# Optimization experiments

Measured on AMD Instinct MI355X. Metric: run time of the kernel, lower is better.

The kernel has to match this reference:

```python
import jax, jax.numpy as jnp
import numpy as np

N = 50000      # nodes
E = 800000     # edges (avg degree 16)
IN = 128       # in_features
OUT = 64       # out_features
NEG_SLOPE = 0.2


def setup_inputs() -> dict:
    key = jax.random.key(0)
    ks = jax.random.split(key, 6)
    x = jax.random.normal(ks[0], (N, IN), dtype=jnp.float32)
    edge_src = jax.random.randint(ks[1], (E,), 0, N, dtype=jnp.int32)  # row i of adj
    edge_dst = jax.random.randint(ks[2], (E,), 0, N, dtype=jnp.int32)  # col j of adj
    stdv = 1.0 / np.sqrt(OUT)
    W = jax.random.uniform(ks[3], (IN, OUT), jnp.float32, -stdv, stdv)
    a = jax.random.uniform(ks[4], (2 * OUT, 1), jnp.float32, -stdv, stdv)
    bias = jax.random.uniform(ks[5], (OUT,), jnp.float32, -stdv, stdv)
    return {"x": x, "W": W, "a": a, "bias": bias,
            "edge_src": edge_src, "edge_dst": edge_dst}


def reference(x, W, a, bias, edge_src, edge_dst):
    # h = input @ weight + bias    [N, OUT]
    h = x @ W + bias
    # Per-node attention halves: Wh1[i] + Wh2[j] == (e = Wh1 + Wh2.T)[i, j]
    Wh1 = h @ a[:OUT, 0]   # [N]
    Wh2 = h @ a[OUT:, 0]   # [N]
    # Edge-centric scores only where adj is nonzero (mirrors e.sparse_mask(adj))
    e = jax.nn.leaky_relu(Wh1[edge_src] + Wh2[edge_dst], NEG_SLOPE)  # [E]
    # Sparse softmax over dim=1 -> segment softmax grouped by source row
    emax = jax.ops.segment_max(e, edge_src, num_segments=N)          # [N]
    ex = jnp.exp(e - emax[edge_src])                                 # [E]
    denom = jax.ops.segment_sum(ex, edge_src, num_segments=N)        # [N]
    alpha = ex / denom[edge_src]                                     # [E]
    # out[i] = sum_j alpha_ij * h[j]  (sparse attention @ h)
    out = jax.ops.segment_sum(alpha[:, None] * h[edge_dst], edge_src,
                              num_segments=N)                        # [N, OUT]
    return out
```

## Files before the change

### kernel.cpp

```cpp
#include <hip/hip_runtime.h>
#include <math.h>


typedef unsigned long long u64;
typedef unsigned int u32;
typedef unsigned short u16;
typedef __attribute__((ext_vector_type(8))) short bf16x8;
typedef __attribute__((ext_vector_type(4))) float f32x4;

namespace {
constexpr int NN   = 50000;
constexpr int EE   = 800000;
constexpr int INF_ = 128;
constexpr int OUTF = 64;
constexpr float NEG_SLOPE = 0.2f;
constexpr int MAXDEG = 64;

constexpr int NBUCK   = 196;
constexpr int BSTRIDE = 16;
constexpr int BCAP    = 4608;
constexpr int S1_CHUNK  = 2048;
constexpr int S1_BLOCKS = (EE + S1_CHUNK - 1) / S1_CHUNK;
constexpr int GEMM_BLOCKS = (NN + 127) / 128;
constexpr int K1_BLOCKS = S1_BLOCKS + GEMM_BLOCKS;
constexpr int AGG_BLOCKS = (NN + 63) / 64;
}

static __device__ __forceinline__ u16 bf16rne(float v) {
    u32 u = __builtin_bit_cast(u32, v);
    return (u16)((u + 0x7fffu + ((u >> 16) & 1u)) >> 16);
}
static __device__ __forceinline__ float bf2f(u16 b) {
    return __builtin_bit_cast(float, (u32)b << 16);
}
static __device__ __forceinline__ u32 pack2bf(float a, float b) {
    return (u32)bf16rne(a) | ((u32)bf16rne(b) << 16);
}

__global__ __launch_bounds__(256)
void gat_fused(const float* __restrict__ x, const float* __restrict__ W,
               const float* __restrict__ av, const float* __restrict__ bias,
               const int* __restrict__ esrc, const int* __restrict__ edst,
               u32* __restrict__ h16, float* __restrict__ wh1,
               float* __restrict__ wh2, int* __restrict__ bcnt_g,
               u64* __restrict__ bdata)
{
    __shared__ u64 smem[4096];
    const int id  = blockIdx.x;
    const int tid = threadIdx.x;
    const int ridx = id >> 1;
    const bool is_gemm = (id & 1) == 0;

    if (!is_gemm) {
        u64* s_pairs = smem;
        int* s_bcnt  = (int*)((char*)smem + 16384);
        int* s_scan  = s_bcnt + NBUCK;
        int* s_goff  = s_scan + NBUCK;

        for (int i = tid; i < NBUCK; i += 256) s_bcnt[i] = 0;
        __syncthreads();

        const int e0  = ridx * S1_CHUNK;
        const int tot = (EE - e0) < S1_CHUNK ? (EE - e0) : S1_CHUNK;

        int mb[8], mp[8]; u64 mv[8]; int nmine = 0;
#pragma unroll
        for (int k = 0; k < 8; ++k) {
            const int e = e0 + tid + k * 256;
            if (e < e0 + tot) {
                const int s = esrc[e], d = edst[e];
                const int b = s >> 8;
                mb[nmine] = b;
                mp[nmine] = atomicAdd(&s_bcnt[b], 1);
                mv[nmine] = ((u64)(u32)d << 32) | (u32)s;
                ++nmine;
            }
        }
        __syncthreads();
        if (tid < NBUCK) s_scan[tid] = s_bcnt[tid];
        __syncthreads();
        for (int off = 1; off < NBUCK; off <<= 1) {
            int v = 0;
            if (tid < NBUCK && tid >= off) v = s_scan[tid - off];
            __syncthreads();
            if (tid < NBUCK && tid >= off) s_scan[tid] += v;
            __syncthreads();
        }
        if (tid < NBUCK) {
            const int c = s_bcnt[tid];
            s_goff[tid] = c > 0 ? atomicAdd(&bcnt_g[tid * BSTRIDE], c) : 0;
        }
        __syncthreads();
        for (int k = 0; k < nmine; ++k) {
            const int b = mb[k];
            s_pairs[s_scan[b] - s_bcnt[b] + mp[k]] = mv[k];
        }
        __syncthreads();
        for (int i = tid; i < tot; i += 256) {
            const u64 p = s_pairs[i];
            const int s = (int)(u32)(p & 0xffffffffull);
            const int b = s >> 8;
            const int g = s_goff[b] + (i - (s_scan[b] - s_bcnt[b]));
            if (g < BCAP) bdata[(size_t)b * BCAP + g] = p;
        }
        return;
    }

    u32* Whi = (u32*)smem;
    u32* Wlo = Whi + 4096;

#pragma unroll
    for (int i = 0; i < 4; ++i) {
        const int idx    = tid * 4 + i;
        const int lane_s = idx & 63;
        const int kt_s   = (idx >> 6) & 3;
        const int nt_s   = idx >> 8;
        const int n  = nt_s * 16 + (lane_s & 15);
        const int k0 = kt_s * 32 + (lane_s >> 4) * 8;
        u32 hw[4], lw[4];
#pragma unroll
        for (int jp = 0; jp < 4; ++jp) {
            const float va = W[(k0 + 2*jp    ) * OUTF + n];
            const float vb = W[(k0 + 2*jp + 1) * OUTF + n];
            const u16 hA = bf16rne(va); const u16 lA = bf16rne(va - bf2f(hA));
            const u16 hB = bf16rne(vb); const u16 lB = bf16rne(vb - bf2f(hB));
            hw[jp] = (u32)hA | ((u32)hB << 16);
            lw[jp] = (u32)lA | ((u32)lB << 16);
        }
        const int off = ((nt_s * 4 + kt_s) * 64 + lane_s) * 4;
        *(uint4*)&Whi[off] = make_uint4(hw[0], hw[1], hw[2], hw[3]);
        *(uint4*)&Wlo[off] = make_uint4(lw[0], lw[1], lw[2], lw[3]);
    }
    __syncthreads();

    const int lane = tid & 63;
    const int w    = tid >> 6;
    const int n15  = lane & 15;
    const int quad = lane >> 4;
    const int node0  = ridx * 128;
    const int nodeA0 = node0 + w * 32;

    f32x4 acc[2][4];
#pragma unroll
    for (int mt = 0; mt < 2; ++mt)
#pragma unroll
        for (int nt = 0; nt < 4; ++nt) acc[mt][nt] = (f32x4)(0.f);

    for (int kt = 0; kt < 4; ++kt) {
        bf16x8 Ahi[2], Alo[2];
#pragma unroll
        for (int mt = 0; mt < 2; ++mt) {
            const int node = nodeA0 + mt * 16 + n15;
            float v[8] = {0.f,0.f,0.f,0.f,0.f,0.f,0.f,0.f};
            if (node < NN) {
                const float4* xr = (const float4*)(x + (size_t)node * INF_ + kt * 32 + quad * 8);
                const float4 p = xr[0], q = xr[1];
                v[0]=p.x; v[1]=p.y; v[2]=p.z; v[3]=p.w;
                v[4]=q.x; v[5]=q.y; v[6]=q.z; v[7]=q.w;
            }
#pragma unroll
            for (int j = 0; j < 8; ++j) {
                const u16 hb = bf16rne(v[j]);
                const u16 lb = bf16rne(v[j] - bf2f(hb));
                Ahi[mt][j] = (short)hb;
                Alo[mt][j] = (short)lb;
            }
        }
#pragma unroll
        for (int nt = 0; nt < 4; ++nt) {
            const int off = ((nt * 4 + kt) * 64 + lane) * 4;
            const bf16x8 Bhi = *(const bf16x8*)&Whi[off];
            const bf16x8 Blo = *(const bf16x8*)&Wlo[off];
#pragma unroll
            for (int mt = 0; mt < 2; ++mt) {
                acc[mt][nt] = __builtin_amdgcn_mfma_f32_16x16x32_bf16(Ahi[mt], Bhi, acc[mt][nt], 0, 0, 0);
                acc[mt][nt] = __builtin_amdgcn_mfma_f32_16x16x32_bf16(Ahi[mt], Blo, acc[mt][nt], 0, 0, 0);
                acc[mt][nt] = __builtin_amdgcn_mfma_f32_16x16x32_bf16(Alo[mt], Bhi, acc[mt][nt], 0, 0, 0);
            }
        }
    }

#pragma unroll
    for (int mt = 0; mt < 2; ++mt) {
        float p1[4] = {0.f,0.f,0.f,0.f}, p2[4] = {0.f,0.f,0.f,0.f};
        float hv[4][4];
#pragma unroll
        for (int nt = 0; nt < 4; ++nt) {
            const int feat = nt * 16 + n15;
            const float bv = bias[feat];
            const float A1 = av[feat];
            const float A2 = av[OUTF + feat];
#pragma unroll
            for (int r = 0; r < 4; ++r) {
                const float d = acc[mt][nt][r] + bv;
                hv[nt][r] = d;
                p1[r] += d * A1;
                p2[r] += d * A2;
            }
        }
#pragma unroll
        for (int r = 0; r < 4; ++r) {
            p1[r] += __shfl_xor(p1[r], 1); p1[r] += __shfl_xor(p1[r], 2);
            p1[r] += __shfl_xor(p1[r], 4); p1[r] += __shfl_xor(p1[r], 8);
            p2[r] += __shfl_xor(p2[r], 1); p2[r] += __shfl_xor(p2[r], 2);
            p2[r] += __shfl_xor(p2[r], 4); p2[r] += __shfl_xor(p2[r], 8);
        }
#pragma unroll
        for (int r = 0; r < 4; ++r) {
            float pk[4];
#pragma unroll
            for (int nt = 0; nt < 4; ++nt) pk[nt] = __shfl_xor(hv[nt][r], 1);
            const int node = nodeA0 + mt * 16 + quad * 4 + r;
            if (node < NN) {
                if ((n15 & 1) == 0) {
#pragma unroll
                    for (int nt = 0; nt < 4; ++nt)
                        h16[(size_t)node * 32 + nt * 8 + (n15 >> 1)] =
                            pack2bf(hv[nt][r], pk[nt]);
                }
                if (n15 == 0) { wh1[node] = p1[r]; wh2[node] = p2[r]; }
            }
        }
    }
}

__global__ __launch_bounds__(256)
void gat_agg(const int* __restrict__ bcnt_g, const u64* __restrict__ bdata,
             const float* __restrict__ wh1, const float* __restrict__ wh2,
             const u32* __restrict__ h16, float* __restrict__ out)
{
    __shared__ int   l_dst[64 * 64];
    __shared__ float l_alpha[64 * 64];
    __shared__ int   l_cnt[64];
    const int tid    = threadIdx.x;
    const int bid    = blockIdx.x;
    const int node0  = bid << 6;
    const int bucket = bid >> 2;

    if (tid < 64) l_cnt[tid] = 0;
    __syncthreads();

    int n = bcnt_g[bucket * BSTRIDE];
    n = n > BCAP ? BCAP : n;
    for (int i = tid; i < n; i += 256) {
        const u64 p = bdata[(size_t)bucket * BCAP + i];
        const int s  = (int)(u32)(p & 0xffffffffull);
        const int ln = s - node0;
        if (ln >= 0 && ln < 64) {
            const int pos = atomicAdd(&l_cnt[ln], 1);
            if (pos < MAXDEG) l_dst[(ln << 6) + pos] = (int)(u32)(p >> 32);
        }
    }
    __syncthreads();

    const int lane = tid & 63;
    const int qw   = (tid >> 6) * 4 + (lane >> 4);
    const int f    = lane & 15;

#pragma unroll
    for (int nl = 0; nl < 4; ++nl) {
        const int li   = qw + 16 * nl;
        const int node = node0 + li;
        int deg = l_cnt[li];
        deg = deg > MAXDEG ? MAXDEG : deg;
        const float w1 = (node < NN) ? wh1[node] : 0.f;

        float el[4]; int dl[4];
        float m = -INFINITY;
#pragma unroll
        for (int k = 0; k < 4; ++k) {
            const int slot = f + 16 * k;
            int d = l_dst[(li << 6) + slot];
            d = (slot < deg) ? d : 0;
            dl[k] = d;
            float v = w1 + wh2[d];
            v = v > 0.f ? v : NEG_SLOPE * v;
            el[k] = (slot < deg) ? v : -INFINITY;
            m = fmaxf(m, el[k]);
        }
        m = fmaxf(m, __shfl_xor(m, 1)); m = fmaxf(m, __shfl_xor(m, 2));
        m = fmaxf(m, __shfl_xor(m, 4)); m = fmaxf(m, __shfl_xor(m, 8));
        float ex[4], s = 0.f;
#pragma unroll
        for (int k = 0; k < 4; ++k) {
            ex[k] = (f + 16 * k < deg) ? __expf(el[k] - m) : 0.f;
            s += ex[k];
        }
        s += __shfl_xor(s, 1); s += __shfl_xor(s, 2);
        s += __shfl_xor(s, 4); s += __shfl_xor(s, 8);
        const float inv = (deg > 0) ? 1.f / s : 0.f;
#pragma unroll
        for (int k = 0; k < 4; ++k) {
            l_alpha[(li << 6) + f + 16 * k] = ex[k] * inv;
            l_dst  [(li << 6) + f + 16 * k] = dl[k];
        }
    }
    __syncthreads();

#pragma unroll
    for (int nl = 0; nl < 4; ++nl) {
        const int li   = qw + 16 * nl;
        const int node = node0 + li;
        int deg = l_cnt[li];
        deg = deg > MAXDEG ? MAXDEG : deg;
        const int base = li << 6;
        float4 acc = make_float4(0.f, 0.f, 0.f, 0.f);
        for (int j0 = 0; j0 < deg; j0 += 8) {
            float aa[8]; int dd[8]; uint2 vv[8];
#pragma unroll
            for (int k = 0; k < 8; ++k) {
                aa[k] = l_alpha[base + j0 + k];
                dd[k] = l_dst[base + j0 + k];
            }
#pragma unroll
            for (int k = 0; k < 8; ++k)
                vv[k] = *(const uint2*)&h16[(size_t)dd[k] * 32 + f * 2];
#define BF_LO(u) __builtin_bit_cast(float, (u) << 16)
#define BF_HI(u) __builtin_bit_cast(float, (u) & 0xffff0000u)
#pragma unroll
            for (int k = 0; k < 8; ++k) {
                acc.x += aa[k] * BF_LO(vv[k].x);
                acc.y += aa[k] * BF_HI(vv[k].x);
                acc.z += aa[k] * BF_LO(vv[k].y);
                acc.w += aa[k] * BF_HI(vv[k].y);
            }
#undef BF_LO
#undef BF_HI
        }
        if (node < NN)
            *(float4*)&out[(size_t)node * OUTF + f * 4] = acc;
    }
}

extern "C" void kernel_launch(void* const* d_in, const int* in_sizes, int n_in,
                              void* d_out, int out_size, void* d_ws, size_t ws_size,
                              hipStream_t stream)
{
    const float* x    = (const float*)d_in[0];
    const float* W    = (const float*)d_in[1];
    const float* av   = (const float*)d_in[2];
    const float* bias = (const float*)d_in[3];
    const int*   esrc = (const int*)d_in[4];
    const int*   edst = (const int*)d_in[5];
    float* out = (float*)d_out;

    u32*   h16    = (u32*)d_ws;
    float* wh1    = (float*)(h16 + (size_t)NN * 32);
    float* wh2    = wh1 + NN;
    int*   bcnt_g = (int*)(wh2 + NN);
    u64*   bdata  = (u64*)(bcnt_g + NBUCK * BSTRIDE + 64);

    hipMemsetAsync(bcnt_g, 0, NBUCK * BSTRIDE * sizeof(int), stream);
    gat_fused<<<K1_BLOCKS, 256, 0, stream>>>(
        x, W, av, bias, esrc, edst, h16, wh1, wh2, bcnt_g, bdata);
    gat_agg<<<AGG_BLOCKS, 256, 0, stream>>>(bcnt_g, bdata, wh1, wh2, h16, out);
}
```

Measured before the change: 121.9 us.

## Precompute split-bf16 W in prep kernel, pack alpha/dst, widen agg gathers

A small prep kernel now zeroes the bucket counters in place of the memset and converts W into hi/lo bf16 fragments once in global memory. The GEMM blocks then read B fragments straight from global/L2 instead of rebuilding them in LDS, which shrinks the shared allocation and should raise occupancy. The aggregation kernel packs alpha and destination index into one u64 per edge with a padded stride to avoid bank conflicts. It also gathers 16-byte h rows per lane, with two lane halves splitting the edges and combining through a shuffle. The risks are an extra launch and repeated global fragment loads inside the GEMM loop.

Result: no change. 123.2 us (+1.0%).

```diff
diff --git a/kernel.cpp b/kernel.cpp
--- a/kernel.cpp
+++ b/kernel.cpp
@@ -38,14 +38,45 @@
 }
 
 __global__ __launch_bounds__(256)
-void gat_fused(const float* __restrict__ x, const float* __restrict__ W,
+void gat_prep(const float* __restrict__ W, int* __restrict__ bcnt_g,
+              u32* __restrict__ Whi_g, u32* __restrict__ Wlo_g)
+{
+    const int tid = threadIdx.x;
+    if (blockIdx.x == 0) {
+        for (int i = tid; i < NBUCK * BSTRIDE; i += 256) bcnt_g[i] = 0;
+        return;
+    }
+    const int idx    = (blockIdx.x - 1) * 256 + tid;
+    const int lane_s = idx & 63;
+    const int kt_s   = (idx >> 6) & 3;
+    const int nt_s   = idx >> 8;
+    const int n  = nt_s * 16 + (lane_s & 15);
+    const int k0 = kt_s * 32 + (lane_s >> 4) * 8;
+    u32 hw[4], lw[4];
+#pragma unroll
+    for (int jp = 0; jp < 4; ++jp) {
+        const float va = W[(k0 + 2*jp    ) * OUTF + n];
+        const float vb = W[(k0 + 2*jp + 1) * OUTF + n];
+        const u16 hA = bf16rne(va); const u16 lA = bf16rne(va - bf2f(hA));
+        const u16 hB = bf16rne(vb); const u16 lB = bf16rne(vb - bf2f(hB));
+        hw[jp] = (u32)hA | ((u32)hB << 16);
+        lw[jp] = (u32)lA | ((u32)lB << 16);
+    }
+    const int off = ((nt_s * 4 + kt_s) * 64 + lane_s) * 4;
+    *(uint4*)&Whi_g[off] = make_uint4(hw[0], hw[1], hw[2], hw[3]);
+    *(uint4*)&Wlo_g[off] = make_uint4(lw[0], lw[1], lw[2], lw[3]);
+}
+
+__global__ __launch_bounds__(256)
+void gat_fused(const float* __restrict__ x,
+               const u32* __restrict__ Whi_g, const u32* __restrict__ Wlo_g,
                const float* __restrict__ av, const float* __restrict__ bias,
                const int* __restrict__ esrc, const int* __restrict__ edst,
                u32* __restrict__ h16, float* __restrict__ wh1,
                float* __restrict__ wh2, int* __restrict__ bcnt_g,
                u64* __restrict__ bdata)
 {
-    __shared__ u64 smem[4096];
+    __shared__ u64 smem[2368];
     const int id  = blockIdx.x;
     const int tid = threadIdx.x;
     const int ridx = id >> 1;
@@ -106,33 +137,6 @@
         return;
     }
 
-    u32* Whi = (u32*)smem;
-    u32* Wlo = Whi + 4096;
-
-#pragma unroll
-    for (int i = 0; i < 4; ++i) {
-        const int idx    = tid * 4 + i;
-        const int lane_s = idx & 63;
-        const int kt_s   = (idx >> 6) & 3;
-        const int nt_s   = idx >> 8;
-        const int n  = nt_s * 16 + (lane_s & 15);
-        const int k0 = kt_s * 32 + (lane_s >> 4) * 8;
-        u32 hw[4], lw[4];
-#pragma unroll
-        for (int jp = 0; jp < 4; ++jp) {
-            const float va = W[(k0 + 2*jp    ) * OUTF + n];
-            const float vb = W[(k0 + 2*jp + 1) * OUTF + n];
-            const u16 hA = bf16rne(va); const u16 lA = bf16rne(va - bf2f(hA));
-            const u16 hB = bf16rne(vb); const u16 lB = bf16rne(vb - bf2f(hB));
-            hw[jp] = (u32)hA | ((u32)hB << 16);
-            lw[jp] = (u32)lA | ((u32)lB << 16);
-        }
-        const int off = ((nt_s * 4 + kt_s) * 64 + lane_s) * 4;
-        *(uint4*)&Whi[off] = make_uint4(hw[0], hw[1], hw[2], hw[3]);
-        *(uint4*)&Wlo[off] = make_uint4(lw[0], lw[1], lw[2], lw[3]);
-    }
-    __syncthreads();
-
     const int lane = tid & 63;
     const int w    = tid >> 6;
     const int n15  = lane & 15;
@@ -169,8 +173,8 @@
 #pragma unroll
         for (int nt = 0; nt < 4; ++nt) {
             const int off = ((nt * 4 + kt) * 64 + lane) * 4;
-            const bf16x8 Bhi = *(const bf16x8*)&Whi[off];
-            const bf16x8 Blo = *(const bf16x8*)&Wlo[off];
+            const bf16x8 Bhi = *(const bf16x8*)&Whi_g[off];
+            const bf16x8 Blo = *(const bf16x8*)&Wlo_g[off];
 #pragma unroll
             for (int mt = 0; mt < 2; ++mt) {
                 acc[mt][nt] = __builtin_amdgcn_mfma_f32_16x16x32_bf16(Ahi[mt], Bhi, acc[mt][nt], 0, 0, 0);
@@ -229,9 +233,8 @@
              const float* __restrict__ wh1, const float* __restrict__ wh2,
              const u32* __restrict__ h16, float* __restrict__ out)
 {
-    __shared__ int   l_dst[64 * 64];
-    __shared__ float l_alpha[64 * 64];
-    __shared__ int   l_cnt[64];
+    __shared__ u64 l_ad[64 * 65];
+    __shared__ int l_cnt[64];
     const int tid    = threadIdx.x;
     const int bid    = blockIdx.x;
     const int node0  = bid << 6;
@@ -248,7 +251,8 @@
         const int ln = s - node0;
         if (ln >= 0 && ln < 64) {
             const int pos = atomicAdd(&l_cnt[ln], 1);
-            if (pos < MAXDEG) l_dst[(ln << 6) + pos] = (int)(u32)(p >> 32);
+            if (pos < MAXDEG)
+                ((u32*)&l_ad[ln * 65 + pos])[1] = (u32)(p >> 32);
         }
     }
     __syncthreads();
@@ -270,7 +274,7 @@
 #pragma unroll
         for (int k = 0; k < 4; ++k) {
             const int slot = f + 16 * k;
-            int d = l_dst[(li << 6) + slot];
+            int d = (int)((u32*)&l_ad[li * 65 + slot])[1];
             d = (slot < deg) ? d : 0;
             dl[k] = d;
             float v = w1 + wh2[d];
@@ -291,44 +295,50 @@
         const float inv = (deg > 0) ? 1.f / s : 0.f;
 #pragma unroll
         for (int k = 0; k < 4; ++k) {
-            l_alpha[(li << 6) + f + 16 * k] = ex[k] * inv;
-            l_dst  [(li << 6) + f + 16 * k] = dl[k];
+            const u32 ab = __builtin_bit_cast(u32, ex[k] * inv);
+            l_ad[li * 65 + f + 16 * k] = (u64)ab | ((u64)(u32)dl[k] << 32);
         }
     }
     __syncthreads();
 
+    const int c  = f & 7;
+    const int eh = f >> 3;
 #pragma unroll
     for (int nl = 0; nl < 4; ++nl) {
         const int li   = qw + 16 * nl;
         const int node = node0 + li;
         int deg = l_cnt[li];
         deg = deg > MAXDEG ? MAXDEG : deg;
-        const int base = li << 6;
-        float4 acc = make_float4(0.f, 0.f, 0.f, 0.f);
-        for (int j0 = 0; j0 < deg; j0 += 8) {
-            float aa[8]; int dd[8]; uint2 vv[8];
+        const int base = li * 65;
+        float a8[8] = {0.f,0.f,0.f,0.f,0.f,0.f,0.f,0.f};
+        for (int j0 = 0; j0 < deg; j0 += 16) {
+            u64 ad[8]; uint4 vv[8];
+#pragma unroll
+            for (int k = 0; k < 8; ++k)
+                ad[k] = l_ad[base + j0 + 2 * k + eh];
 #pragma unroll
             for (int k = 0; k < 8; ++k) {
-                aa[k] = l_alpha[base + j0 + k];
-                dd[k] = l_dst[base + j0 + k];
-            }
-#pragma unroll
-            for (int k = 0; k < 8; ++k)
-                vv[k] = *(const uint2*)&h16[(size_t)dd[k] * 32 + f * 2];
+                const u32 d = (u32)(ad[k] >> 32);
+                vv[k] = *(const uint4*)&h16[(size_t)d * 32 + c * 4];
+            }
 #define BF_LO(u) __builtin_bit_cast(float, (u) << 16)
 #define BF_HI(u) __builtin_bit_cast(float, (u) & 0xffff0000u)
 #pragma unroll
             for (int k = 0; k < 8; ++k) {
-                acc.x += aa[k] * BF_LO(vv[k].x);
-                acc.y += aa[k] * BF_HI(vv[k].x);
-                acc.z += aa[k] * BF_LO(vv[k].y);
-                acc.w += aa[k] * BF_HI(vv[k].y);
+                const float a = __builtin_bit_cast(float, (u32)ad[k]);
+                a8[0] += a * BF_LO(vv[k].x); a8[1] += a * BF_HI(vv[k].x);
+                a8[2] += a * BF_LO(vv[k].y); a8[3] += a * BF_HI(vv[k].y);
+                a8[4] += a * BF_LO(vv[k].z); a8[5] += a * BF_HI(vv[k].z);
+                a8[6] += a * BF_LO(vv[k].w); a8[7] += a * BF_HI(vv[k].w);
             }
 #undef BF_LO
 #undef BF_HI
         }
+#pragma unroll
+        for (int i = 0; i < 8; ++i) a8[i] += __shfl_xor(a8[i], 8);
         if (node < NN)
-            *(float4*)&out[(size_t)node * OUTF + f * 4] = acc;
+            *(float4*)&out[(size_t)node * OUTF + c * 8 + eh * 4] =
+                make_float4(a8[eh*4+0], a8[eh*4+1], a8[eh*4+2], a8[eh*4+3]);
     }
 }
 
@@ -348,10 +358,12 @@
     float* wh1    = (float*)(h16 + (size_t)NN * 32);
     float* wh2    = wh1 + NN;
     int*   bcnt_g = (int*)(wh2 + NN);
-    u64*   bdata  = (u64*)(bcnt_g + NBUCK * BSTRIDE + 64);
-
-    hipMemsetAsync(bcnt_g, 0, NBUCK * BSTRIDE * sizeof(int), stream);
+    u32*   Whi_g  = (u32*)(bcnt_g + NBUCK * BSTRIDE);
+    u32*   Wlo_g  = Whi_g + 4096;
+    u64*   bdata  = (u64*)(Wlo_g + 4096);
+
+    gat_prep<<<5, 256, 0, stream>>>(W, bcnt_g, Whi_g, Wlo_g);
     gat_fused<<<K1_BLOCKS, 256, 0, stream>>>(
-        x, W, av, bias, esrc, edst, h16, wh1, wh2, bcnt_g, bdata);
+        x, Whi_g, Wlo_g, av, bias, esrc, edst, h16, wh1, wh2, bcnt_g, bdata);
     gat_agg<<<AGG_BLOCKS, 256, 0, stream>>>(bcnt_g, bdata, wh1, wh2, h16, out);
 }
```
